# Kernel optimization log

Measured on AMD Instinct MI355X. Metric: run time of the kernel, lower is better.

## Reference

```python
import jax, jax.numpy as jnp
import numpy as np

K = 3          # cfg.KNN_UP
CHUNK = 2048   # point chunk for brute-force KNN
BN_EPS = 1e-5


def knn_interp(vox_c, vox_f, pt_c):
    """Inverse-distance k-NN interpolation of voxel features onto points.
    vox_c: [Nv,3] voxel centers; vox_f: [Nv,C]; pt_c: [Np,3]. Returns [Np,C]."""
    Np = pt_c.shape[0]

    def chunk_fn(pc):  # pc: [CHUNK,3]
        d2 = jnp.sum((pc[:, None, :] - vox_c[None, :, :]) ** 2, axis=-1)  # [CHUNK,Nv]
        neg_d2, idx = jax.lax.top_k(-d2, K)                               # k nearest
        d = jnp.sqrt(jnp.maximum(-neg_d2, 0.0))
        w = 1.0 / (d + 1e-8)
        w = w / jnp.sum(w, axis=-1, keepdims=True)                        # [CHUNK,K]
        return jnp.sum(vox_f[idx] * w[..., None], axis=1)                 # [CHUNK,C]

    out = jax.lax.map(chunk_fn, pt_c.reshape(Np // CHUNK, CHUNK, 3))
    return out.reshape(Np, vox_f.shape[-1])


def bn1d(x, gamma, beta):
    # BatchNorm1d in training mode, applied per decomposed batch item (as in
    # the original per-sample list comprehension): stats over the point dim.
    mu = jnp.mean(x, axis=0, keepdims=True)
    var = jnp.var(x, axis=0, keepdims=True)
    return gamma * (x - mu) * jax.lax.rsqrt(var + BN_EPS) + beta


def level_forward(vox_c, vox_f, pt_c, gamma, beta):
    f = jax.vmap(knn_interp, in_axes=(0, 0, 0))(vox_c, vox_f, pt_c)  # [B,Np,C]
    return jax.vmap(lambda xf: bn1d(xf, gamma, beta))(f)


def setup_inputs() -> dict:
    key = jax.random.key(0)
    ks = jax.random.split(key, 16)
    B, Np = 2, 32768
    SCENE = 50.0  # spread coordinates over a ~50m scene
    nvs = [2048, 6144, 16384, 32768]
    chs = [256, 128, 96, 96]
    inp = {"pt_c": jax.random.uniform(ks[0], (B, Np, 3), jnp.float32) * SCENE}
    for i, (nv, c) in enumerate(zip(nvs, chs), start=1):
        inp[f"vox_c{i}"] = jax.random.uniform(ks[2 * i - 1], (B, nv, 3), jnp.float32) * SCENE
        inp[f"vox_f{i}"] = jax.random.normal(ks[2 * i], (B, nv, c), jnp.float32)
        inp[f"gamma{i}"] = jnp.ones((c,), jnp.float32)
        inp[f"beta{i}"] = jnp.zeros((c,), jnp.float32)
    return inp


def reference(pt_c, vox_c1, vox_f1, gamma1, beta1,
              vox_c2, vox_f2, gamma2, beta2,
              vox_c3, vox_f3, gamma3, beta3,
              vox_c4, vox_f4, gamma4, beta4):
    # voxel_to_point: per-level KNN upsampling of decoder voxel features to
    # the raw point cloud, followed by per-sample BatchNorm1d.
    f1 = level_forward(vox_c1, vox_f1, pt_c, gamma1, beta1)
    f2 = level_forward(vox_c2, vox_f2, pt_c, gamma2, beta2)
    f3 = level_forward(vox_c3, vox_f3, pt_c, gamma3, beta3)
    f4 = level_forward(vox_c4, vox_f4, pt_c, gamma4, beta4)
    return (f1, f2, f3, f4)
```

## Files before the change

### kernel.cpp

```cpp
#include <hip/hip_runtime.h>
#include <cfloat>
#include <climits>
#include <cstdint>

#define NPOINTS 32768
#define NBATCH  2
#define NLEV    4
#define NPB     128
#define NBLK    (NPOINTS / NPB)

struct Level {
  const float4* sorted;
  const int*    start;
  int*          idxo;
  float*        wo;
  int G, ncells, Nv;
  float h, invh;
};
struct Params { Level lv[NLEV]; };

__device__ __forceinline__ int cell1d(float x, float invh, int G) {
  int c = (int)(x * invh);
  return min(max(c, 0), G - 1);
}

__global__ __launch_bounds__(256) void zero_kernel(int* __restrict__ p, int n)
{
  int i = blockIdx.x * 256 + threadIdx.x;
  if (i < n) p[i] = 0;
}

__global__ __launch_bounds__(256) void count_kernel(
    const float* __restrict__ voxc, int* __restrict__ cnt,
    int Nv, int G, float invh, int ncells)
{
  int v = blockIdx.x * 256 + threadIdx.x;
  int b = blockIdx.y;
  if (v >= Nv) return;
  const float* p = voxc + ((size_t)b * Nv + v) * 3;
  int cx = cell1d(p[0], invh, G), cy = cell1d(p[1], invh, G), cz = cell1d(p[2], invh, G);
  atomicAdd(&cnt[b * ncells + (cz * G + cy) * G + cx], 1);
}

__global__ __launch_bounds__(1024) void scan_kernel(
    const int* __restrict__ cnt, int* __restrict__ start, int* __restrict__ cur,
    int ncells)
{
  const int b = blockIdx.x, t = threadIdx.x;
  const int* c  = cnt + (size_t)b * ncells;
  int* st = start + (size_t)b * (ncells + 1);
  int* cu = cur + (size_t)b * ncells;
  __shared__ int part[1024];
  const int chunk = (ncells + 1023) / 1024;
  const int lo = t * chunk, hi = min(lo + chunk, ncells);
  int s = 0;
  for (int i = lo; i < hi; ++i) s += c[i];
  part[t] = s;
  __syncthreads();
  for (int off = 1; off < 1024; off <<= 1) {
    int v = (t >= off) ? part[t - off] : 0;
    __syncthreads();
    part[t] += v;
    __syncthreads();
  }
  int base = (t > 0) ? part[t - 1] : 0;
  for (int i = lo; i < hi; ++i) { st[i] = base; cu[i] = base; base += c[i]; }
  if (t == 1023) st[ncells] = part[1023];
}

__global__ __launch_bounds__(256) void scatter_kernel(
    const float* __restrict__ voxc, int* __restrict__ cur,
    float4* __restrict__ sorted, int Nv, int G, float invh, int ncells)
{
  int v = blockIdx.x * 256 + threadIdx.x;
  int b = blockIdx.y;
  if (v >= Nv) return;
  const float* p = voxc + ((size_t)b * Nv + v) * 3;
  float x = p[0], y = p[1], z = p[2];
  int cx = cell1d(x, invh, G), cy = cell1d(y, invh, G), cz = cell1d(z, invh, G);
  int pos = atomicAdd(&cur[b * ncells + (cz * G + cy) * G + cx], 1);
  sorted[(size_t)b * Nv + pos] = make_float4(x, y, z, __int_as_float(v));
}

__global__ __launch_bounds__(256) void query_kernel(
    const float* __restrict__ ptc, Params prm)
{
  const int l = blockIdx.y, b = blockIdx.z;
  const Level L = prm.lv[l];
  const int tid = threadIdx.x;
  const int q = tid & 3;
  const int p = blockIdx.x * 64 + (tid >> 2);
  const float* pp = ptc + ((size_t)b * NPOINTS + p) * 3;
  const float px = pp[0], py = pp[1], pz = pp[2];
  const int G = L.G;
  const float h = L.h;

  const int cx = cell1d(px, L.invh, G);
  const int cy = cell1d(py, L.invh, G);
  const int cz = cell1d(pz, L.invh, G);
  const float fx = px - cx * h, fy = py - cy * h, fz = pz - cz * h;
  float m = fminf(fminf(fminf(fx, h - fx), fminf(fy, h - fy)), fminf(fz, h - fz));
  m = fmaxf(m, 0.f);

  const int* start     = L.start  + (size_t)b * (L.ncells + 1);
  const float4* sorted = L.sorted + (size_t)b * L.Nv;

  float b0 = FLT_MAX, b1 = FLT_MAX, b2 = FLT_MAX;
  int   i0 = INT_MAX, i1 = INT_MAX, i2 = INT_MAX;

  auto ins = [&](float d2, int vi) {
    if (d2 < b2 || (d2 == b2 && vi < i2)) {
      if (d2 < b1 || (d2 == b1 && vi < i1)) {
        b2 = b1; i2 = i1;
        if (d2 < b0 || (d2 == b0 && vi < i0)) { b1 = b0; i1 = i0; b0 = d2; i0 = vi; }
        else                                  { b1 = d2; i1 = vi; }
      } else { b2 = d2; i2 = vi; }
    }
  };
  auto cand = [&](int k) {
    float4 vv = sorted[k];
    int vi = __float_as_int(vv.w);
    float dx = px - vv.x, dy = py - vv.y, dz = pz - vv.z;
    float d2 = __fadd_rn(__fadd_rn(__fmul_rn(dx, dx), __fmul_rn(dy, dy)),
                         __fmul_rn(dz, dz));
    ins(d2, vi);
  };
  auto scan_range = [&](int ks, int ke) {
    for (int k = ks + q; k < ke; k += 4) cand(k);
  };

  const int rmax = max(max(cx, G - 1 - cx), max(max(cy, G - 1 - cy), max(cz, G - 1 - cz)));
  for (int rho = 0; rho <= rmax; ++rho) {
    if (rho >= 1) {
      float bm = fminf(b2, __shfl_xor(b2, 1));
      bm = fminf(bm, __shfl_xor(bm, 2));
      float dmin = fmaxf((rho - 1) * h + m, 0.f);
      if (dmin * dmin * 0.99999f > bm) break;
    }
    const int z0 = max(cz - rho, 0), z1 = min(cz + rho, G - 1);
    const int y0 = max(cy - rho, 0), y1 = min(cy + rho, G - 1);
    for (int iz = z0; iz <= z1; ++iz) {
      const int adz = abs(iz - cz);
      for (int iy = y0; iy <= y1; ++iy) {
        const int ady = max(adz, abs(iy - cy));
        const int row = (iz * G + iy) * G;
        if (ady == rho) {
          const int x0 = max(cx - rho, 0), x1 = min(cx + rho, G - 1);
          scan_range(start[row + x0], start[row + x1 + 1]);
        } else {
          const int xl = cx - rho, xr = cx + rho;
          if (xl >= 0)     scan_range(start[row + xl], start[row + xl + 1]);
          if (xr <= G - 1) scan_range(start[row + xr], start[row + xr + 1]);
        }
      }
    }
  }

  #pragma unroll
  for (int mask = 1; mask <= 2; mask <<= 1) {
    float c0 = __shfl_xor(b0, mask), c1 = __shfl_xor(b1, mask), c2 = __shfl_xor(b2, mask);
    int   j0 = __shfl_xor(i0, mask), j1 = __shfl_xor(i1, mask), j2 = __shfl_xor(i2, mask);
    ins(c0, j0); ins(c1, j1); ins(c2, j2);
  }

  if (q == 0) {
    float w0 = 1.0f / (sqrtf(b0) + 1e-8f);
    float w1 = 1.0f / (sqrtf(b1) + 1e-8f);
    float w2 = 1.0f / (sqrtf(b2) + 1e-8f);
    float ws = (w0 + w1) + w2;
    size_t o = ((size_t)b * NPOINTS + p) * 3;
    L.idxo[o] = i0; L.idxo[o + 1] = i1; L.idxo[o + 2] = i2;
    L.wo[o] = w0 / ws; L.wo[o + 1] = w1 / ws; L.wo[o + 2] = w2 / ws;
  }
}

template <int C, int BDIM>
__global__ __launch_bounds__(BDIM) void interp_kernel(
    const float* __restrict__ voxf, const int* __restrict__ idxo,
    const float* __restrict__ wo, float* __restrict__ out,
    float* __restrict__ psum, float* __restrict__ psq, int Nv)
{
  constexpr int C4 = C / 4;
  constexpr int R  = BDIM / C4;
  const int b = blockIdx.y, blk = blockIdx.x;
  const int tid = threadIdx.x;
  const int r = tid / C4, c4 = tid - r * C4;
  const float4* fb = (const float4*)(voxf + (size_t)b * Nv * C);
  float4* ob = (float4*)(out + (size_t)b * NPOINTS * C);
  const int p0 = blk * NPB;

  float4 s = make_float4(0, 0, 0, 0), q = make_float4(0, 0, 0, 0);
  for (int p = p0 + r; p < p0 + NPB; p += R) {
    size_t pg = ((size_t)b * NPOINTS + p) * 3;
    int   ia = idxo[pg], ib = idxo[pg + 1], ic = idxo[pg + 2];
    float wa = wo[pg],   wb = wo[pg + 1],   wc = wo[pg + 2];
    float4 fa = fb[(size_t)ia * C4 + c4];
    float4 f2 = fb[(size_t)ib * C4 + c4];
    float4 fc = fb[(size_t)ic * C4 + c4];
    float4 o;
    o.x = wa * fa.x + wb * f2.x + wc * fc.x;
    o.y = wa * fa.y + wb * f2.y + wc * fc.y;
    o.z = wa * fa.z + wb * f2.z + wc * fc.z;
    o.w = wa * fa.w + wb * f2.w + wc * fc.w;
    ob[(size_t)p * C4 + c4] = o;
    s.x += o.x; s.y += o.y; s.z += o.z; s.w += o.w;
    q.x += o.x * o.x; q.y += o.y * o.y; q.z += o.z * o.z; q.w += o.w * o.w;
  }

  __shared__ float4 ls[BDIM];
  ls[tid] = s;
  __syncthreads();
  if (r == 0) {
    float4 tot = s;
    #pragma unroll
    for (int rr = 1; rr < R; ++rr) {
      float4 v = ls[c4 + rr * C4];
      tot.x += v.x; tot.y += v.y; tot.z += v.z; tot.w += v.w;
    }
    ((float4*)psum)[((size_t)b * NBLK + blk) * C4 + c4] = tot;
  }
  __syncthreads();
  ls[tid] = q;
  __syncthreads();
  if (r == 0) {
    float4 tot = q;
    #pragma unroll
    for (int rr = 1; rr < R; ++rr) {
      float4 v = ls[c4 + rr * C4];
      tot.x += v.x; tot.y += v.y; tot.z += v.z; tot.w += v.w;
    }
    ((float4*)psq)[((size_t)b * NBLK + blk) * C4 + c4] = tot;
  }
}

__global__ __launch_bounds__(256) void bn_stats_kernel(
    const float* __restrict__ psum, const float* __restrict__ psq,
    const float* __restrict__ gamma, const float* __restrict__ beta,
    float* __restrict__ scale, float* __restrict__ shift, int C, float invN)
{
  const int c = blockIdx.x, b = blockIdx.y, t = threadIdx.x;
  float s = 0.f, q = 0.f;
  for (int k = t; k < NBLK; k += 256) {
    s += psum[((size_t)b * NBLK + k) * C + c];
    q += psq[((size_t)b * NBLK + k) * C + c];
  }
  __shared__ float ss[256], qs[256];
  ss[t] = s; qs[t] = q;
  __syncthreads();
  for (int o = 128; o > 0; o >>= 1) {
    if (t < o) { ss[t] += ss[t + o]; qs[t] += qs[t + o]; }
    __syncthreads();
  }
  if (t == 0) {
    float mu  = ss[0] * invN;
    float var = fmaxf(qs[0] * invN - mu * mu, 0.f);
    float sc  = gamma[c] * rsqrtf(var + 1e-5f);
    scale[b * C + c] = sc;
    shift[b * C + c] = beta[c] - mu * sc;
  }
}

__global__ __launch_bounds__(256) void bn_apply_kernel(
    float* __restrict__ out, const float* __restrict__ scale,
    const float* __restrict__ shift, int C, int NpC)
{
  const int e = blockIdx.x * 256 + threadIdx.x;
  const int npc4 = NpC >> 2, c4n = C >> 2;
  const int b = e / npc4;
  const int rem = e - b * npc4;
  const int c4 = rem % c4n;
  float4 v  = ((float4*)out)[e];
  float4 sc = ((const float4*)scale)[b * c4n + c4];
  float4 sh = ((const float4*)shift)[b * c4n + c4];
  v.x = fmaf(v.x, sc.x, sh.x);
  v.y = fmaf(v.y, sc.y, sh.y);
  v.z = fmaf(v.z, sc.z, sh.z);
  v.w = fmaf(v.w, sc.w, sh.w);
  ((float4*)out)[e] = v;
}

extern "C" void kernel_launch(void* const* d_in, const int* in_sizes, int n_in,
                              void* d_out, int out_size, void* d_ws, size_t ws_size,
                              hipStream_t stream)
{
  const float* ptc = (const float*)d_in[0];
  static const int    Cs[4]     = {256, 128, 96, 96};
  static const int    Nvs[4]    = {2048, 6144, 16384, 32768};
  static const int    Gs[4]     = {10, 14, 18, 22};
  static const size_t outOff[4] = {0, 16777216, 25165824, 31457280};

  size_t off = 0;
  auto carve = [&](size_t bytes) {
    off = (off + 255) & ~(size_t)255;
    size_t o = off; off += bytes; return o;
  };
  float4* sorted[4]; int* cnt[4]; int* stt[4]; int* cur[4];
  int nc[4];
  char* w = (char*)d_ws;
  for (int l = 0; l < 4; ++l) {
    nc[l] = Gs[l] * Gs[l] * Gs[l];
    sorted[l] = (float4*)(w + carve((size_t)NBATCH * Nvs[l] * 16));
    cnt[l]    = (int*)   (w + carve((size_t)NBATCH * nc[l] * 4));
    stt[l]    = (int*)   (w + carve((size_t)NBATCH * (nc[l] + 1) * 4));
    cur[l]    = (int*)   (w + carve((size_t)NBATCH * nc[l] * 4));
  }
  int*   idxo  = (int*)  (w + carve((size_t)NLEV * NBATCH * NPOINTS * 3 * 4));
  float* wo    = (float*)(w + carve((size_t)NLEV * NBATCH * NPOINTS * 3 * 4));
  float* psum  = (float*)(w + carve((size_t)NBATCH * NBLK * 256 * 4));
  float* psq   = (float*)(w + carve((size_t)NBATCH * NBLK * 256 * 4));
  float* scale = (float*)(w + carve((size_t)NBATCH * 256 * 4));
  float* shift = (float*)(w + carve((size_t)NBATCH * 256 * 4));

  Params prm;
  for (int l = 0; l < 4; ++l) {
    Level& L = prm.lv[l];
    L.sorted = sorted[l]; L.start = stt[l];
    L.idxo = idxo + (size_t)l * NBATCH * NPOINTS * 3;
    L.wo   = wo   + (size_t)l * NBATCH * NPOINTS * 3;
    L.G = Gs[l]; L.ncells = nc[l]; L.Nv = Nvs[l];
    L.h = 50.0f / Gs[l]; L.invh = Gs[l] / 50.0f;
  }

  for (int l = 0; l < 4; ++l) {
    const float* voxc = (const float*)d_in[1 + 4 * l];
    zero_kernel<<<(NBATCH * nc[l] + 255) / 256, 256, 0, stream>>>(cnt[l], NBATCH * nc[l]);
    count_kernel<<<dim3((Nvs[l] + 255) / 256, NBATCH), 256, 0, stream>>>(
        voxc, cnt[l], Nvs[l], Gs[l], prm.lv[l].invh, nc[l]);
    scan_kernel<<<NBATCH, 1024, 0, stream>>>(cnt[l], stt[l], cur[l], nc[l]);
    scatter_kernel<<<dim3((Nvs[l] + 255) / 256, NBATCH), 256, 0, stream>>>(
        voxc, cur[l], sorted[l], Nvs[l], Gs[l], prm.lv[l].invh, nc[l]);
  }

  query_kernel<<<dim3(NPOINTS / 64, NLEV, NBATCH), 256, 0, stream>>>(ptc, prm);

  for (int l = 0; l < 4; ++l) {
    const float* voxf  = (const float*)d_in[2 + 4 * l];
    const float* gamma = (const float*)d_in[3 + 4 * l];
    const float* beta  = (const float*)d_in[4 + 4 * l];
    const int C = Cs[l], Nv = Nvs[l];
    float* outl = (float*)d_out + outOff[l];
    const int* idl = idxo + (size_t)l * NBATCH * NPOINTS * 3;
    const float* wl = wo  + (size_t)l * NBATCH * NPOINTS * 3;

    if (C == 256)
      interp_kernel<256, 256><<<dim3(NBLK, NBATCH), 256, 0, stream>>>(
          voxf, idl, wl, outl, psum, psq, Nv);
    else if (C == 128)
      interp_kernel<128, 256><<<dim3(NBLK, NBATCH), 256, 0, stream>>>(
          voxf, idl, wl, outl, psum, psq, Nv);
    else
      interp_kernel<96, 240><<<dim3(NBLK, NBATCH), 240, 0, stream>>>(
          voxf, idl, wl, outl, psum, psq, Nv);

    bn_stats_kernel<<<dim3(C, NBATCH), 256, 0, stream>>>(
        psum, psq, gamma, beta, scale, shift, C, 1.0f / NPOINTS);

    const int n4 = NBATCH * NPOINTS * C / 4;
    bn_apply_kernel<<<n4 / 256, 256, 0, stream>>>(
        (float*)outl, scale, shift, C, NPOINTS * C);
  }
}
```

Measured before the change: 389.7 us.

## Batch binning launches across levels and spatially sort query points for locality

Merges the four per-level zero/count/scan/scatter launch sequences into one set of launches indexed by a job dimension, which cuts about twelve kernel launches. It also adds a fifth binning job that sorts the query points on a 16^3 grid. The query kernel then reads points in spatial order, so neighbouring threads touch nearby voxel cells, improving cache locality and reducing divergence. The cost is an extra sort of 32768 points per batch, and output writes are now scattered through the original point index.

```diff
diff --git a/kernel.cpp b/kernel.cpp
--- a/kernel.cpp
+++ b/kernel.cpp
@@ -6,8 +6,20 @@
 #define NPOINTS 32768
 #define NBATCH  2
 #define NLEV    4
+#define NJOB    5
+#define PG      16
+#define PCELLS  (PG*PG*PG)
 #define NPB     128
 #define NBLK    (NPOINTS / NPB)
+
+struct BinJob {
+  const float* coords;
+  int* cnt; int* start; int* cur;
+  float4* sorted;
+  int G, ncells, N;
+  float invh;
+};
+struct BinParams { BinJob job[NJOB]; };
 
 struct Level {
   const float4* sorted;
@@ -30,26 +42,25 @@
   if (i < n) p[i] = 0;
 }
 
-__global__ __launch_bounds__(256) void count_kernel(
-    const float* __restrict__ voxc, int* __restrict__ cnt,
-    int Nv, int G, float invh, int ncells)
-{
+__global__ __launch_bounds__(256) void count_kernel(BinParams prm)
+{
+  const BinJob J = prm.job[blockIdx.z];
   int v = blockIdx.x * 256 + threadIdx.x;
   int b = blockIdx.y;
-  if (v >= Nv) return;
-  const float* p = voxc + ((size_t)b * Nv + v) * 3;
-  int cx = cell1d(p[0], invh, G), cy = cell1d(p[1], invh, G), cz = cell1d(p[2], invh, G);
-  atomicAdd(&cnt[b * ncells + (cz * G + cy) * G + cx], 1);
-}
-
-__global__ __launch_bounds__(1024) void scan_kernel(
-    const int* __restrict__ cnt, int* __restrict__ start, int* __restrict__ cur,
-    int ncells)
-{
+  if (v >= J.N) return;
+  const float* p = J.coords + ((size_t)b * J.N + v) * 3;
+  int cx = cell1d(p[0], J.invh, J.G), cy = cell1d(p[1], J.invh, J.G), cz = cell1d(p[2], J.invh, J.G);
+  atomicAdd(&J.cnt[b * J.ncells + (cz * J.G + cy) * J.G + cx], 1);
+}
+
+__global__ __launch_bounds__(1024) void scan_kernel(BinParams prm)
+{
+  const BinJob J = prm.job[blockIdx.y];
   const int b = blockIdx.x, t = threadIdx.x;
-  const int* c  = cnt + (size_t)b * ncells;
-  int* st = start + (size_t)b * (ncells + 1);
-  int* cu = cur + (size_t)b * ncells;
+  const int ncells = J.ncells;
+  const int* c  = J.cnt + (size_t)b * ncells;
+  int* st = J.start + (size_t)b * (ncells + 1);
+  int* cu = J.cur + (size_t)b * ncells;
   __shared__ int part[1024];
   const int chunk = (ncells + 1023) / 1024;
   const int lo = t * chunk, hi = min(lo + chunk, ncells);
@@ -68,30 +79,30 @@
   if (t == 1023) st[ncells] = part[1023];
 }
 
-__global__ __launch_bounds__(256) void scatter_kernel(
-    const float* __restrict__ voxc, int* __restrict__ cur,
-    float4* __restrict__ sorted, int Nv, int G, float invh, int ncells)
-{
+__global__ __launch_bounds__(256) void scatter_kernel(BinParams prm)
+{
+  const BinJob J = prm.job[blockIdx.z];
   int v = blockIdx.x * 256 + threadIdx.x;
   int b = blockIdx.y;
-  if (v >= Nv) return;
-  const float* p = voxc + ((size_t)b * Nv + v) * 3;
+  if (v >= J.N) return;
+  const float* p = J.coords + ((size_t)b * J.N + v) * 3;
   float x = p[0], y = p[1], z = p[2];
-  int cx = cell1d(x, invh, G), cy = cell1d(y, invh, G), cz = cell1d(z, invh, G);
-  int pos = atomicAdd(&cur[b * ncells + (cz * G + cy) * G + cx], 1);
-  sorted[(size_t)b * Nv + pos] = make_float4(x, y, z, __int_as_float(v));
+  int cx = cell1d(x, J.invh, J.G), cy = cell1d(y, J.invh, J.G), cz = cell1d(z, J.invh, J.G);
+  int pos = atomicAdd(&J.cur[b * J.ncells + (cz * J.G + cy) * J.G + cx], 1);
+  J.sorted[(size_t)b * J.N + pos] = make_float4(x, y, z, __int_as_float(v));
 }
 
 __global__ __launch_bounds__(256) void query_kernel(
-    const float* __restrict__ ptc, Params prm)
+    const float4* __restrict__ psorted, Params prm)
 {
   const int l = blockIdx.y, b = blockIdx.z;
   const Level L = prm.lv[l];
   const int tid = threadIdx.x;
   const int q = tid & 3;
-  const int p = blockIdx.x * 64 + (tid >> 2);
-  const float* pp = ptc + ((size_t)b * NPOINTS + p) * 3;
-  const float px = pp[0], py = pp[1], pz = pp[2];
+  const int sp = blockIdx.x * 64 + (tid >> 2);
+  float4 pt = psorted[(size_t)b * NPOINTS + sp];
+  const float px = pt.x, py = pt.y, pz = pt.z;
+  const int p = __float_as_int(pt.w);
   const int G = L.G;
   const float h = L.h;
 
@@ -294,15 +305,30 @@
     off = (off + 255) & ~(size_t)255;
     size_t o = off; off += bytes; return o;
   };
-  float4* sorted[4]; int* cnt[4]; int* stt[4]; int* cur[4];
-  int nc[4];
   char* w = (char*)d_ws;
-  for (int l = 0; l < 4; ++l) {
-    nc[l] = Gs[l] * Gs[l] * Gs[l];
-    sorted[l] = (float4*)(w + carve((size_t)NBATCH * Nvs[l] * 16));
-    cnt[l]    = (int*)   (w + carve((size_t)NBATCH * nc[l] * 4));
-    stt[l]    = (int*)   (w + carve((size_t)NBATCH * (nc[l] + 1) * 4));
-    cur[l]    = (int*)   (w + carve((size_t)NBATCH * nc[l] * 4));
+
+  int nc[NJOB];
+  for (int l = 0; l < 4; ++l) nc[l] = Gs[l] * Gs[l] * Gs[l];
+  nc[4] = PCELLS;
+  int Ns[NJOB] = {Nvs[0], Nvs[1], Nvs[2], Nvs[3], NPOINTS};
+  int Gj[NJOB] = {Gs[0], Gs[1], Gs[2], Gs[3], PG};
+
+  int totcnt = 0;
+  for (int j = 0; j < NJOB; ++j) totcnt += nc[j];
+  int* cntbase = (int*)(w + carve((size_t)NBATCH * totcnt * 4));
+
+  float4* sortedj[NJOB]; int* cntj[NJOB]; int* sttj[NJOB]; int* curj[NJOB];
+  {
+    int acc = 0;
+    for (int j = 0; j < NJOB; ++j) {
+      cntj[j] = cntbase + (size_t)NBATCH * acc;
+      acc += nc[j];
+    }
+  }
+  for (int j = 0; j < NJOB; ++j) {
+    sortedj[j] = (float4*)(w + carve((size_t)NBATCH * Ns[j] * 16));
+    sttj[j]    = (int*)   (w + carve((size_t)NBATCH * (nc[j] + 1) * 4));
+    curj[j]    = (int*)   (w + carve((size_t)NBATCH * nc[j] * 4));
   }
   int*   idxo  = (int*)  (w + carve((size_t)NLEV * NBATCH * NPOINTS * 3 * 4));
   float* wo    = (float*)(w + carve((size_t)NLEV * NBATCH * NPOINTS * 3 * 4));
@@ -311,27 +337,32 @@
   float* scale = (float*)(w + carve((size_t)NBATCH * 256 * 4));
   float* shift = (float*)(w + carve((size_t)NBATCH * 256 * 4));
 
+  BinParams bp;
+  for (int j = 0; j < NJOB; ++j) {
+    BinJob& J = bp.job[j];
+    J.coords = (j < 4) ? (const float*)d_in[1 + 4 * j] : ptc;
+    J.cnt = cntj[j]; J.start = sttj[j]; J.cur = curj[j]; J.sorted = sortedj[j];
+    J.G = Gj[j]; J.ncells = nc[j]; J.N = Ns[j];
+    J.invh = Gj[j] / 50.0f;
+  }
+
   Params prm;
   for (int l = 0; l < 4; ++l) {
     Level& L = prm.lv[l];
-    L.sorted = sorted[l]; L.start = stt[l];
+    L.sorted = sortedj[l]; L.start = sttj[l];
     L.idxo = idxo + (size_t)l * NBATCH * NPOINTS * 3;
     L.wo   = wo   + (size_t)l * NBATCH * NPOINTS * 3;
     L.G = Gs[l]; L.ncells = nc[l]; L.Nv = Nvs[l];
     L.h = 50.0f / Gs[l]; L.invh = Gs[l] / 50.0f;
   }
 
-  for (int l = 0; l < 4; ++l) {
-    const float* voxc = (const float*)d_in[1 + 4 * l];
-    zero_kernel<<<(NBATCH * nc[l] + 255) / 256, 256, 0, stream>>>(cnt[l], NBATCH * nc[l]);
-    count_kernel<<<dim3((Nvs[l] + 255) / 256, NBATCH), 256, 0, stream>>>(
-        voxc, cnt[l], Nvs[l], Gs[l], prm.lv[l].invh, nc[l]);
-    scan_kernel<<<NBATCH, 1024, 0, stream>>>(cnt[l], stt[l], cur[l], nc[l]);
-    scatter_kernel<<<dim3((Nvs[l] + 255) / 256, NBATCH), 256, 0, stream>>>(
-        voxc, cur[l], sorted[l], Nvs[l], Gs[l], prm.lv[l].invh, nc[l]);
-  }
-
-  query_kernel<<<dim3(NPOINTS / 64, NLEV, NBATCH), 256, 0, stream>>>(ptc, prm);
+  const int zn = NBATCH * totcnt;
+  zero_kernel<<<(zn + 255) / 256, 256, 0, stream>>>(cntbase, zn);
+  count_kernel<<<dim3((NPOINTS + 255) / 256, NBATCH, NJOB), 256, 0, stream>>>(bp);
+  scan_kernel<<<dim3(NBATCH, NJOB), 1024, 0, stream>>>(bp);
+  scatter_kernel<<<dim3((NPOINTS + 255) / 256, NBATCH, NJOB), 256, 0, stream>>>(bp);
+
+  query_kernel<<<dim3(NPOINTS / 64, NLEV, NBATCH), 256, 0, stream>>>(sortedj[4], prm);
 
   for (int l = 0; l < 4; ++l) {
     const float* voxf  = (const float*)d_in[2 + 4 * l];
```

Result: faster. 338.9 us (-13.0%).
